# Optimization experiments

Hardware: AMD Instinct MI355X
Metric: run time of the kernel (lower is better)

Reference implementation:

```python
import jax, jax.numpy as jnp
import numpy as np
from jax import lax

K = 16  # number of KNN neighbors (fixed in module)


def _knn_neighbors(x, k):
    # x: (B, 3, N) point coordinates -> neighbor coords (B, 3, N, K)
    inner = jnp.einsum('bdn,bdm->bnm', x, x)          # (B, N, N)
    sq = jnp.sum(x * x, axis=1)                        # (B, N)
    d2 = sq[:, :, None] + sq[:, None, :] - 2.0 * inner  # pairwise sq dists (B, N, N)
    _, nbr_idx = lax.top_k(-d2, k)                     # k nearest (incl. self), (B, N, K)
    # gather neighbor coordinates: expand x to (B, 3, 1, N), idx to (B, 1, N, K)
    neighbor = jnp.take_along_axis(x[:, :, None, :], nbr_idx[:, None, :, :], axis=3)
    return neighbor  # (B, 3, N, K)


def _down_index(neighbor, x, npts_ds):
    # center-diff saliency: sum of squared offsets to K neighbors per point
    diff = neighbor - x[:, :, :, None]                 # (B, 3, N, K)
    score = jnp.sum(diff * diff, axis=(1, 3))          # (B, N)
    _, idx = lax.top_k(score, npts_ds)                 # (B, npts_ds)
    return idx


def setup_inputs() -> dict:
    key = jax.random.key(0)
    k1, k2 = jax.random.split(key)
    B, N, C = 8, 4096, 128
    x = jax.random.normal(k1, (B, 3, N), dtype=jnp.float32)
    y = jax.random.normal(k2, (B, C, N), dtype=jnp.float32)
    return {"x": x, "y": y, "npts_ds": 2048}


def reference(x, y, npts_ds):
    B, _, N = x.shape
    C = y.shape[1]
    neighbor = _knn_neighbors(x, K)                    # ops.group(x, K, 'neighbor')
    idx = _down_index(neighbor, x, npts_ds)            # ops.down_index(...), (B, npts_ds)
    idx3 = jnp.broadcast_to(idx[:, None, :], (B, 3, npts_ds))
    idxC = jnp.broadcast_to(idx[:, None, :], (B, C, npts_ds))
    top_k_xyz = jnp.take_along_axis(x, idx3, axis=2)    # (B, 3, npts_ds)
    top_k_points = jnp.take_along_axis(y, idxC, axis=2)  # (B, C, npts_ds)
    return (top_k_xyz, top_k_points)
```

## Files before the change

kernel.cpp:

```cpp
#include <hip/hip_runtime.h>
#include <math.h>

#define BATCH 8
#define NPTS 4096
#define CHAN 128
#define KNN 16
#define SPLIT 4
#define CHUNK (NPTS / SPLIT)
#define ISPLIT 2
#define QCH (CHUNK / ISPLIT)
#define RSPLIT 4
#define RCHUNK (NPTS / RSPLIT)

typedef unsigned long long u64;

__device__ __forceinline__ u64 pack_key(float d2, int idx) {
  unsigned b = __float_as_uint(d2);
  b ^= (unsigned)((int)b >> 31) | 0x80000000u;
  return ((u64)b << 32) | (unsigned)idx;
}

__device__ __forceinline__ void ce_asc(u64& x, u64& y) {
  bool sw = y < x;
  u64 lo = sw ? y : x;
  u64 hi = sw ? x : y;
  x = lo;
  y = hi;
}

__device__ __forceinline__ void batcher_sort16(u64 a[16]) {
#define CE(i, j) ce_asc(a[i], a[j])
  CE(0, 8); CE(1, 9); CE(2, 10); CE(3, 11);
  CE(4, 12); CE(5, 13); CE(6, 14); CE(7, 15);
  CE(0, 4); CE(1, 5); CE(2, 6); CE(3, 7);
  CE(8, 12); CE(9, 13); CE(10, 14); CE(11, 15);
  CE(4, 8); CE(5, 9); CE(6, 10); CE(7, 11);
  CE(0, 2); CE(1, 3); CE(4, 6); CE(5, 7);
  CE(8, 10); CE(9, 11); CE(12, 14); CE(13, 15);
  CE(2, 8); CE(3, 9); CE(6, 12); CE(7, 13);
  CE(2, 4); CE(3, 5); CE(6, 8); CE(7, 9); CE(10, 12); CE(11, 13);
  CE(0, 1); CE(2, 3); CE(4, 5); CE(6, 7);
  CE(8, 9); CE(10, 11); CE(12, 13); CE(14, 15);
  CE(1, 8); CE(3, 10); CE(5, 12); CE(7, 14);
  CE(1, 4); CE(3, 6); CE(5, 8); CE(7, 10); CE(9, 12); CE(11, 14);
  CE(1, 2); CE(3, 4); CE(5, 6); CE(7, 8); CE(9, 10); CE(11, 12); CE(13, 14);
#undef CE
}

__device__ __forceinline__ void merge_keep16(u64 T[16], const u64 A[16]) {
  u64 nt[16];
#pragma unroll
  for (int i = 0; i < 16; ++i) {
    u64 a = A[15 - i];
    nt[i] = (a < T[i]) ? a : T[i];
  }
#pragma unroll
  for (int j = 8; j > 0; j >>= 1) {
#pragma unroll
    for (int i = 0; i < 16; ++i) {
      int l = i ^ j;
      if (l > i) ce_asc(nt[i], nt[l]);
    }
  }
#pragma unroll
  for (int i = 0; i < 16; ++i) T[i] = nt[i];
}

__global__ __attribute__((amdgpu_waves_per_eu(4, 4)))
__launch_bounds__(512) void knn_partial_kernel(
    const float* __restrict__ x, u64* __restrict__ pkey) {
  const int s = blockIdx.x % SPLIT;
  const int ntile = (blockIdx.x / SPLIT) % (NPTS / 256);
  const int b = blockIdx.x / (SPLIT * (NPTS / 256));
  const int p = threadIdx.x & 255;
  const int h = threadIdx.x >> 8;
  __shared__ float4 xs[CHUNK];
  __shared__ u64 mbuf[KNN][256];

  const float* xb = x + (size_t)b * 3 * NPTS;
  for (int i = threadIdx.x; i < CHUNK; i += 512) {
    int gm = s * CHUNK + i;
    float px = xb[gm];
    float py = xb[NPTS + gm];
    float pz = xb[2 * NPTS + gm];
    float sq = __fadd_rn(__fadd_rn(__fmul_rn(px, px), __fmul_rn(py, py)),
                         __fmul_rn(pz, pz));
    xs[i] = make_float4(px, py, pz, sq);
  }

  const int n = ntile * 256 + p;
  float ppx = xb[n];
  float ppy = xb[NPTS + n];
  float ppz = xb[2 * NPTS + n];
  float psq = __fadd_rn(__fadd_rn(__fmul_rn(ppx, ppx), __fmul_rn(ppy, ppy)),
                        __fmul_rn(ppz, ppz));
  __syncthreads();

  u64 T[16];
#pragma unroll
  for (int i = 0; i < 16; ++i) T[i] = ~0ull;

  const int cbase = h * QCH;
  for (int base = 0; base < QCH; base += 16) {
    u64 A[16];
#pragma unroll
    for (int t = 0; t < 16; ++t) {
      float4 q = xs[cbase + base + t];
      float inner = __fadd_rn(
          __fadd_rn(__fmul_rn(ppx, q.x), __fmul_rn(ppy, q.y)),
          __fmul_rn(ppz, q.z));
      float d2 = __fsub_rn(__fadd_rn(psq, q.w), __fmul_rn(2.0f, inner));
      A[t] = pack_key(d2, s * CHUNK + cbase + base + t);
    }
    batcher_sort16(A);
    merge_keep16(T, A);
  }

  if (h == 1) {
#pragma unroll
    for (int j = 0; j < 16; ++j) mbuf[j][p] = T[j];
  }
  __syncthreads();
  if (h == 0) {
    u64 A[16];
#pragma unroll
    for (int j = 0; j < 16; ++j) A[j] = mbuf[j][p];
    merge_keep16(T, A);
    u64* pb = pkey + ((size_t)(b * SPLIT + s) * KNN) * NPTS + n;
#pragma unroll
    for (int j = 0; j < 16; ++j) pb[(size_t)j * NPTS] = T[j];
  }
}

__global__ __attribute__((amdgpu_waves_per_eu(1, 2)))
__launch_bounds__(256) void merge_score_kernel(
    const float* __restrict__ x, const u64* __restrict__ pkey,
    float* __restrict__ score, int* __restrict__ cnt) {
  const int b = blockIdx.x / (NPTS / 256);
  const int n = (blockIdx.x % (NPTS / 256)) * 256 + threadIdx.x;

  cnt[(size_t)b * NPTS + n] = 0;

  u64 T[16];
  {
    const u64* pb = pkey + ((size_t)(b * SPLIT + 0) * KNN) * NPTS + n;
#pragma unroll
    for (int j = 0; j < 16; ++j) T[j] = pb[(size_t)j * NPTS];
  }
#pragma unroll
  for (int s = 1; s < SPLIT; ++s) {
    const u64* pb = pkey + ((size_t)(b * SPLIT + s) * KNN) * NPTS + n;
    u64 A[16];
#pragma unroll
    for (int j = 0; j < 16; ++j) A[j] = pb[(size_t)j * NPTS];
    merge_keep16(T, A);
  }

  const float* xb = x + (size_t)b * 3 * NPTS;
  float ppx = xb[n];
  float ppy = xb[NPTS + n];
  float ppz = xb[2 * NPTS + n];

  float nx[KNN], ny[KNN], nz[KNN];
#pragma unroll
  for (int j = 0; j < KNN; ++j) {
    int idx = (int)(unsigned)T[j];
    nx[j] = xb[idx];
    ny[j] = xb[NPTS + idx];
    nz[j] = xb[2 * NPTS + idx];
  }

  float P[3];
#pragma unroll
  for (int d = 0; d < 3; ++d) {
    const float pc = (d == 0) ? ppx : ((d == 1) ? ppy : ppz);
    float r[8];
#pragma unroll
    for (int j = 0; j < 8; ++j) {
      float c0 = (d == 0) ? nx[j] : ((d == 1) ? ny[j] : nz[j]);
      float c1 = (d == 0) ? nx[j + 8] : ((d == 1) ? ny[j + 8] : nz[j + 8]);
      float e0 = __fsub_rn(c0, pc);
      float e1 = __fsub_rn(c1, pc);
      r[j] = __fadd_rn(__fmul_rn(e0, e0), __fmul_rn(e1, e1));
    }
    float t0 = __fadd_rn(r[0], r[1]);
    float t1 = __fadd_rn(r[2], r[3]);
    float t2 = __fadd_rn(r[4], r[5]);
    float t3 = __fadd_rn(r[6], r[7]);
    P[d] = __fadd_rn(__fadd_rn(t0, t1), __fadd_rn(t2, t3));
  }
  score[(size_t)b * NPTS + n] =
      __fadd_rn(__fadd_rn(P[0], P[1]), P[2]);
}

__global__ __launch_bounds__(256) void rank_partial_kernel(
    const float* __restrict__ score, int* __restrict__ cnt) {
  const int s = blockIdx.x % RSPLIT;
  const int ntile = (blockIdx.x / RSPLIT) % (NPTS / 256);
  const int b = blockIdx.x / (RSPLIT * (NPTS / 256));
  __shared__ float ss[RCHUNK];

  const float* sb = score + (size_t)b * NPTS;
  for (int i = threadIdx.x; i < RCHUNK; i += 256)
    ss[i] = sb[s * RCHUNK + i];

  const int n = ntile * 256 + threadIdx.x;
  const float sn = sb[n];
  __syncthreads();

  int c = 0;
#pragma unroll 8
  for (int mm = 0; mm < RCHUNK; ++mm) {
    float sm = ss[mm];
    int gm = s * RCHUNK + mm;
    c += (sm > sn) || (sm == sn && gm < n);
  }
  atomicAdd(&cnt[(size_t)b * NPTS + n], c);
}

__global__ __launch_bounds__(256) void rank_scatter_kernel(
    const int* __restrict__ cnt, int* __restrict__ sel, int npts) {
  int t = blockIdx.x * 256 + threadIdx.x;
  int b = t / NPTS;
  int n = t % NPTS;
  int c = cnt[t];
  if (c < npts) sel[(size_t)b * npts + c] = n;
}

__global__ __launch_bounds__(256) void gather_kernel(
    const float* __restrict__ x, const float* __restrict__ y,
    const int* __restrict__ sel, float* __restrict__ out, int npts,
    int total0, int total) {
  int tid = blockIdx.x * blockDim.x + threadIdx.x;
  if (tid >= total) return;
  if (tid < total0) {
    int j = tid % npts;
    int rest = tid / npts;
    int d = rest % 3;
    int b = rest / 3;
    int src = sel[b * npts + j];
    out[tid] = x[((size_t)b * 3 + d) * NPTS + src];
  } else {
    int t = tid - total0;
    int j = t % npts;
    int rest = t / npts;
    int c = rest % CHAN;
    int b = rest / CHAN;
    int src = sel[b * npts + j];
    out[tid] = y[((size_t)b * CHAN + c) * NPTS + src];
  }
}

extern "C" void kernel_launch(void* const* d_in, const int* in_sizes, int n_in,
                              void* d_out, int out_size, void* d_ws,
                              size_t ws_size, hipStream_t stream) {
  const float* x = (const float*)d_in[0];
  const float* y = (const float*)d_in[1];
  float* out = (float*)d_out;

  const int npts = out_size / (BATCH * (3 + CHAN));

  char* w = (char*)d_ws;
  u64* pkey = (u64*)w;
  w += sizeof(u64) * (size_t)BATCH * SPLIT * KNN * NPTS;
  float* score = (float*)w;
  w += sizeof(float) * (size_t)BATCH * NPTS;
  int* cnt = (int*)w;
  w += sizeof(int) * (size_t)BATCH * NPTS;
  int* sel = (int*)w;

  knn_partial_kernel<<<BATCH * (NPTS / 256) * SPLIT, 512, 0, stream>>>(
      x, pkey);
  merge_score_kernel<<<BATCH * NPTS / 256, 256, 0, stream>>>(x, pkey, score,
                                                             cnt);
  rank_partial_kernel<<<BATCH * (NPTS / 256) * RSPLIT, 256, 0, stream>>>(
      score, cnt);
  rank_scatter_kernel<<<BATCH * NPTS / 256, 256, 0, stream>>>(cnt, sel, npts);

  const int total0 = BATCH * 3 * npts;
  gather_kernel<<<(out_size + 255) / 256, 256, 0, stream>>>(
      x, y, sel, out, npts, total0, out_size);
}
```

Measured before the change: 294.7 us.

## Two-pass KNN: 32-bit distance threshold, then collect and sort candidate keys

The per-point top-16 selection in the KNN partial kernel now sorts and merges 32-bit distance bit patterns instead of packed 64-bit distance/index keys, which yields a threshold equal to the 16th-smallest distance. A second pass recomputes the distances, stores the indices of candidates at or below the threshold in a per-thread shared buffer capped at 24 entries, and finishes with a 32-element bitonic sort on packed 64-bit keys. The goal is to cut the cost of the compare-exchange network in the hot loop by halving key width. In exchange it adds a second distance pass and 24KB of shared memory. Candidates can be silently dropped if more than 24 tie at the threshold.

Measured after the change: 268.3 us. 1.1x faster.

```diff
diff --git a/kernel.cpp b/kernel.cpp
--- a/kernel.cpp
+++ b/kernel.cpp
@@ -9,6 +9,7 @@
 #define CHUNK (NPTS / SPLIT)
 #define ISPLIT 2
 #define QCH (CHUNK / ISPLIT)
+#define PCAP 24
 #define RSPLIT 4
 #define RCHUNK (NPTS / RSPLIT)
 
@@ -18,6 +19,13 @@
   unsigned b = __float_as_uint(d2);
   b ^= (unsigned)((int)b >> 31) | 0x80000000u;
   return ((u64)b << 32) | (unsigned)idx;
+}
+
+__device__ __forceinline__ float d2_ref(float4 q, float ppx, float ppy,
+                                        float ppz, float psq) {
+  float inner = __fadd_rn(__fadd_rn(__fmul_rn(ppx, q.x), __fmul_rn(ppy, q.y)),
+                          __fmul_rn(ppz, q.z));
+  return __fsub_rn(__fadd_rn(psq, q.w), __fmul_rn(2.0f, inner));
 }
 
 __device__ __forceinline__ void ce_asc(u64& x, u64& y) {
@@ -28,8 +36,51 @@
   y = hi;
 }
 
-__device__ __forceinline__ void batcher_sort16(u64 a[16]) {
-#define CE(i, j) ce_asc(a[i], a[j])
+__device__ __forceinline__ void bitonic_sort32(u64 a[32]) {
+#pragma unroll
+  for (int k = 2; k <= 32; k <<= 1) {
+#pragma unroll
+    for (int j = k >> 1; j > 0; j >>= 1) {
+#pragma unroll
+      for (int i = 0; i < 32; ++i) {
+        int l = i ^ j;
+        if (l > i) {
+          if ((i & k) == 0) ce_asc(a[i], a[l]);
+          else              ce_asc(a[l], a[i]);
+        }
+      }
+    }
+  }
+}
+
+__device__ __forceinline__ void merge_keep16(u64 T[16], const u64 A[16]) {
+  u64 nt[16];
+#pragma unroll
+  for (int i = 0; i < 16; ++i) {
+    u64 a = A[15 - i];
+    nt[i] = (a < T[i]) ? a : T[i];
+  }
+#pragma unroll
+  for (int j = 8; j > 0; j >>= 1) {
+#pragma unroll
+    for (int i = 0; i < 16; ++i) {
+      int l = i ^ j;
+      if (l > i) ce_asc(nt[i], nt[l]);
+    }
+  }
+#pragma unroll
+  for (int i = 0; i < 16; ++i) T[i] = nt[i];
+}
+
+__device__ __forceinline__ void ce_i32(int& x, int& y) {
+  int lo = (x < y) ? x : y;
+  int hi = (x < y) ? y : x;
+  x = lo;
+  y = hi;
+}
+
+__device__ __forceinline__ void batcher_sort16_i32(int a[16]) {
+#define CE(i, j) ce_i32(a[i], a[j])
   CE(0, 8); CE(1, 9); CE(2, 10); CE(3, 11);
   CE(4, 12); CE(5, 13); CE(6, 14); CE(7, 15);
   CE(0, 4); CE(1, 5); CE(2, 6); CE(3, 7);
@@ -47,11 +98,11 @@
 #undef CE
 }
 
-__device__ __forceinline__ void merge_keep16(u64 T[16], const u64 A[16]) {
-  u64 nt[16];
+__device__ __forceinline__ void merge_keep16_i32(int T[16], const int A[16]) {
+  int nt[16];
 #pragma unroll
   for (int i = 0; i < 16; ++i) {
-    u64 a = A[15 - i];
+    int a = A[15 - i];
     nt[i] = (a < T[i]) ? a : T[i];
   }
 #pragma unroll
@@ -59,7 +110,7 @@
 #pragma unroll
     for (int i = 0; i < 16; ++i) {
       int l = i ^ j;
-      if (l > i) ce_asc(nt[i], nt[l]);
+      if (l > i) ce_i32(nt[i], nt[l]);
     }
   }
 #pragma unroll
@@ -75,6 +126,7 @@
   const int p = threadIdx.x & 255;
   const int h = threadIdx.x >> 8;
   __shared__ float4 xs[CHUNK];
+  __shared__ unsigned short idxbuf[512 * PCAP];
   __shared__ u64 mbuf[KNN][256];
 
   const float* xb = x + (size_t)b * 3 * NPTS;
@@ -96,39 +148,65 @@
                         __fmul_rn(ppz, ppz));
   __syncthreads();
 
-  u64 T[16];
-#pragma unroll
-  for (int i = 0; i < 16; ++i) T[i] = ~0ull;
-
   const int cbase = h * QCH;
+
+  int T[16];
+#pragma unroll
+  for (int i = 0; i < 16; ++i) T[i] = 0x7FFFFFFF;
+
   for (int base = 0; base < QCH; base += 16) {
-    u64 A[16];
+    int A[16];
 #pragma unroll
     for (int t = 0; t < 16; ++t) {
       float4 q = xs[cbase + base + t];
-      float inner = __fadd_rn(
-          __fadd_rn(__fmul_rn(ppx, q.x), __fmul_rn(ppy, q.y)),
-          __fmul_rn(ppz, q.z));
-      float d2 = __fsub_rn(__fadd_rn(psq, q.w), __fmul_rn(2.0f, inner));
-      A[t] = pack_key(d2, s * CHUNK + cbase + base + t);
-    }
-    batcher_sort16(A);
-    merge_keep16(T, A);
-  }
+      A[t] = __float_as_int(d2_ref(q, ppx, ppy, ppz, psq));
+    }
+    batcher_sort16_i32(A);
+    merge_keep16_i32(T, A);
+  }
+  const int v15 = T[15];
+
+  unsigned short* mybuf = &idxbuf[(unsigned)threadIdx.x * PCAP];
+  int cnt = 0;
+#pragma unroll 4
+  for (int m = 0; m < QCH; ++m) {
+    float4 q = xs[cbase + m];
+    int bits = __float_as_int(d2_ref(q, ppx, ppy, ppz, psq));
+    if (bits <= v15) {
+      mybuf[cnt < PCAP - 1 ? cnt : PCAP - 1] = (unsigned short)(cbase + m);
+      ++cnt;
+    }
+  }
+
+  u64 K[32];
+#pragma unroll
+  for (int j = 0; j < PCAP; ++j) {
+    int loc = mybuf[j] & (CHUNK - 1);
+    float4 q = xs[loc];
+    float d2 = d2_ref(q, ppx, ppy, ppz, psq);
+    u64 k = pack_key(d2, s * CHUNK + loc);
+    K[j] = (j < cnt) ? k : ~0ull;
+  }
+#pragma unroll
+  for (int j = PCAP; j < 32; ++j) K[j] = ~0ull;
+  bitonic_sort32(K);
 
   if (h == 1) {
 #pragma unroll
-    for (int j = 0; j < 16; ++j) mbuf[j][p] = T[j];
+    for (int j = 0; j < 16; ++j) mbuf[j][p] = K[j];
   }
   __syncthreads();
   if (h == 0) {
-    u64 A[16];
-#pragma unroll
-    for (int j = 0; j < 16; ++j) A[j] = mbuf[j][p];
-    merge_keep16(T, A);
+    u64 T64[16];
+#pragma unroll
+    for (int j = 0; j < 16; ++j) T64[j] = K[j];
+    u64 A64[16];
+#pragma unroll
+    for (int j = 0; j < 16; ++j) A64[j] = mbuf[j][p];
+    merge_keep16(T64, A64);
     u64* pb = pkey + ((size_t)(b * SPLIT + s) * KNN) * NPTS + n;
 #pragma unroll
-    for (int j = 0; j < 16; ++j) pb[(size_t)j * NPTS] = T[j];
+    for (int j = 0; j < 16; ++j) pb[(size_t)j * NPTS] = T64[j];
   }
 }
 
```
